# Optimization experiments

Hardware: AMD Instinct MI355X
Metric: run time of the kernel (lower is better)

Reference implementation:

```python
import jax, jax.numpy as jnp
import numpy as np

V_EN = 50000; V_FR = 50000; D = 256; B = 64; S = 64; NEG = 8192; PAD = 0


def setup_inputs() -> dict:
    key = jax.random.key(0)
    k = jax.random.split(key, 8)
    zs = jax.random.normal(k[0], (B, S, D), dtype=jnp.float32) * 0.1
    x_en = jax.random.randint(k[1], (B, S), 1, V_EN)  # avoid pad row 0
    x_fr = jax.random.randint(k[2], (B, S), 1, V_FR)
    en_mask = jnp.ones((B, S), dtype=jnp.float32)
    fr_mask = jnp.ones((B, S), dtype=jnp.float32)
    W_en = jax.random.normal(k[3], (V_EN, D), dtype=jnp.float32) * 0.05
    W_en = W_en.at[PAD].set(0.0)  # padding_idx row is zero
    W_fr = jax.random.normal(k[4], (V_FR, D), dtype=jnp.float32) * 0.05
    W_fr = W_fr.at[PAD].set(0.0)
    # Host-side CSS sampling, mirroring the torch module's numpy/multinomial step.
    rng = np.random.default_rng(0)
    pos_en = np.unique(np.asarray(x_en))
    neg_en = rng.choice(np.setdiff1d(np.arange(V_EN), pos_en), NEG, replace=False)
    kappa_en = jnp.float32((V_EN - pos_en.shape[0]) / NEG)
    pos_fr = np.unique(np.asarray(x_fr))
    neg_fr = rng.choice(np.setdiff1d(np.arange(V_FR), pos_fr), NEG, replace=False)
    kappa_fr = jnp.float32((V_FR - pos_fr.shape[0]) / NEG)
    return {
        "zs": zs, "x_en": x_en, "x_fr": x_fr,
        "en_mask": en_mask, "fr_mask": fr_mask,
        "W_en": W_en, "W_fr": W_fr,
        "pos_en": jnp.asarray(pos_en), "neg_en": jnp.asarray(neg_en),
        "pos_fr": jnp.asarray(pos_fr), "neg_fr": jnp.asarray(neg_fr),
        "kappa_en": kappa_en, "kappa_fr": kappa_fr,
    }


def _css_denom(zs, W, pos_idx, neg_idx, kappa):
    # zs: [B,S,D]; pos/neg embeddings: [P,D]/[N,D] -> denom [B,S]
    pos_e = W[pos_idx]
    neg_e = W[neg_idx]
    pos_score = jnp.exp(jnp.einsum("bsd,pd->bsp", zs, pos_e)).sum(-1)
    neg_score = kappa * jnp.exp(jnp.einsum("bsd,nd->bsn", zs, neg_e)).sum(-1)
    return pos_score + neg_score


def reference(zs, x_en, x_fr, en_mask, fr_mask, W_en, W_fr,
              pos_en, neg_en, pos_fr, neg_fr, kappa_en, kappa_fr):
    # --- English CSS: per-token score ---
    be_en = W_en[x_en]                                   # [B,S,D]
    en_batch = jnp.exp((zs * be_en).sum(-1))             # [B,S]
    en_probs = en_batch / _css_denom(zs, W_en, pos_en, neg_en, kappa_en)
    # --- French CSS: alignment score against every en position ---
    be_fr = W_fr[x_fr]                                   # [B,Sf,D]
    fr_batch = jnp.exp(jnp.einsum("bfd,bsd->bfs", be_fr, zs))  # [B,Sf,S]
    fr_denom = _css_denom(zs, W_fr, pos_fr, neg_fr, kappa_fr)  # [B,S]
    fr_probs = fr_batch / fr_denom[:, None, :]
    en_rec_loss = (jnp.log(en_probs) * en_mask).sum(axis=1)            # [B]
    fr_rec_loss = (jnp.log(fr_probs.sum(axis=2)) * fr_mask).sum(axis=1)  # [B]
    return en_rec_loss, fr_rec_loss
```

## Files before the change

### kernel.cpp

```cpp
#include <hip/hip_runtime.h>

#define DDIM 256
#define NTOK 4096
#define NEGN 8192
#define LOG2E 1.4426950408889634f
#define TM 64
#define TN 64
#define LDT 40

typedef __attribute__((ext_vector_type(8))) short bf16x8;
typedef __attribute__((ext_vector_type(4))) float f32x4;

__device__ inline unsigned short f2bf(float f) {
    unsigned int u = __float_as_uint(f);
    unsigned int r = u + 0x7FFFu + ((u >> 16) & 1u);
    return (unsigned short)(r >> 16);
}

__device__ inline float exp2fast(float x) {
    float r;
    asm("v_exp_f32 %0, %1" : "=v"(r) : "v"(x));
    return r;
}

__device__ inline void gl_lds16(const unsigned short* g, unsigned short* l) {
    __builtin_amdgcn_global_load_lds(
        reinterpret_cast<__attribute__((address_space(1))) unsigned int*>(
            reinterpret_cast<uintptr_t>(g)),
        reinterpret_cast<__attribute__((address_space(3))) unsigned int*>(
            reinterpret_cast<uintptr_t>(l)),
        16, 0, 0);
}

__device__ inline void wait_vmcnt0() { asm volatile("s_waitcnt vmcnt(0)" ::: "memory"); }
__device__ inline void raw_barrier() { asm volatile("s_barrier" ::: "memory"); }

template<int CTRL>
__device__ inline float dpp_add(float x) {
    int v = __builtin_amdgcn_update_dpp(0, __float_as_int(x), CTRL, 0xF, 0xF, false);
    return x + __int_as_float(v);
}
__device__ inline float red16(float x) {
    x = dpp_add<0xB1>(x);
    x = dpp_add<0x4E>(x);
    x = dpp_add<0x141>(x);
    x = dpp_add<0x140>(x);
    return x;
}

__global__ void gather_kernel(
    const float* __restrict__ zs,
    const float* __restrict__ W_en, const float* __restrict__ W_fr,
    const int* __restrict__ pos_en, const int* __restrict__ neg_en,
    const int* __restrict__ pos_fr, const int* __restrict__ neg_fr,
    const int* __restrict__ x_en,
    unsigned short* __restrict__ z_bf,
    unsigned short* __restrict__ E_en, unsigned short* __restrict__ E_fr,
    float* __restrict__ en_score,
    float* __restrict__ denom_en, float* __restrict__ denom_fr,
    int Pe, int Pf, int Lpe, int Lpf)
{
    int row  = blockIdx.x * 4 + (threadIdx.x >> 6);
    int lane = threadIdx.x & 63;
    const float* src = nullptr;
    unsigned short* dst = nullptr;
    bool zero = false;
    float sc = LOG2E;

    if (row < NTOK) {
        src = zs + (size_t)row * DDIM;
        dst = z_bf + (size_t)row * DDIM;
        sc = 1.0f;
        if (lane == 0) { denom_en[row] = 0.0f; denom_fr[row] = 0.0f; }
    } else if (row < NTOK + Lpe) {
        int j = row - NTOK;
        int Le = Pe + NEGN;
        int idx = 0;
        if (j < Pe)      idx = pos_en[j];
        else if (j < Le) idx = neg_en[j - Pe];
        else             zero = true;
        src = W_en + (size_t)idx * DDIM;
        dst = E_en + (size_t)j * DDIM;
    } else if (row < NTOK + Lpe + Lpf) {
        int j = row - NTOK - Lpe;
        int Lf = Pf + NEGN;
        int idx = 0;
        if (j < Pf)      idx = pos_fr[j];
        else if (j < Lf) idx = neg_fr[j - Pf];
        else             zero = true;
        src = W_fr + (size_t)idx * DDIM;
        dst = E_fr + (size_t)j * DDIM;
    } else if (row < NTOK + Lpe + Lpf + NTOK) {
        int j = row - NTOK - Lpe - Lpf;
        int idx = x_en[j];
        float4 z = *(const float4*)(zs   + (size_t)j   * DDIM + lane * 4);
        float4 w = *(const float4*)(W_en + (size_t)idx * DDIM + lane * 4);
        float s = z.x * w.x + z.y * w.y + z.z * w.z + z.w * w.w;
        #pragma unroll
        for (int m = 32; m; m >>= 1) s += __shfl_xor(s, m);
        if (lane == 0) en_score[j] = s;
        return;
    } else {
        return;
    }

    int d = lane * 4;
    float4 v;
    if (zero) { v.x = v.y = v.z = v.w = 0.0f; }
    else      { v = *(const float4*)(src + d); }
    ushort4 o;
    o.x = f2bf(v.x * sc); o.y = f2bf(v.y * sc);
    o.z = f2bf(v.z * sc); o.w = f2bf(v.w * sc);
    *(ushort4*)(dst + d) = o;
}

__global__ __launch_bounds__(512, 4) void expsum_stream(
    const unsigned short* __restrict__ A,
    const unsigned short* __restrict__ E,
    const float* __restrict__ kep, const float* __restrict__ kfp,
    float* __restrict__ out_en, float* __restrict__ out_fr,
    int Pe, int Pf, int Lpe, int NT)
{
    __shared__ __align__(16) unsigned short Bs[2][32 * 512];

    int lin = blockIdx.y * 64 + blockIdx.x;
    int xcd = lin & 7;
    int xb  = (lin >> 3) & 15;
    int sl  = xcd + 8 * (lin >> 7);

    int t    = threadIdx.x;
    int lane = t & 63;
    int wave = t >> 6;
    int col  = lane & 15;
    int quad = lane >> 4;

    float ke = kep[0], kf = kfp[0];
    asm volatile("" : "+v"(ke), "+v"(kf) : : "memory");

    bf16x8 afr[2][8];
    {
        const unsigned short* Ap =
            A + ((size_t)(xb * 256 + wave * 32 + col)) * DDIM + quad * 8;
        #pragma unroll
        for (int i = 0; i < 2; i++)
            #pragma unroll
            for (int c = 0; c < 8; c++)
                afr[i][c] = *(const bf16x8*)(Ap + (size_t)i * 16 * DDIM + c * 32);
    }

    float sums[2][4];
    #pragma unroll
    for (int i = 0; i < 2; i++)
        #pragma unroll
        for (int rr = 0; rr < 4; rr++) sums[i][rr] = 0.0f;

    f32x4 accA[2], accB[2];
    #pragma unroll
    for (int i = 0; i < 2; i++) accB[i] = (f32x4){0.f, 0.f, 0.f, 0.f};
    float wjP = 0.0f;
    float* curout = out_en;
    int outrow = xb * 256 + wave * 32;

    int ntiles = (NT - sl + 31) >> 5;

    #define STAGE_TILE(s) do {                                               \
        int tl_ = sl + ((s) << 5);                                           \
        const unsigned short* g_ =                                           \
            E + (size_t)(tl_ * 64 + lane) * DDIM + wave * 32;                \
        unsigned short* l_ = &Bs[(s) & 1][(wave * 4) * 512];                 \
        _Pragma("unroll")                                                    \
        for (int d_ = 0; d_ < 4; d_++)                                       \
            gl_lds16(g_ + d_ * 8, l_ + d_ * 512);                            \
    } while (0)

    #define J_SWEEP(J, ACCC, ACCD, WJD) do {                                 \
        _Pragma("unroll")                                                    \
        for (int i = 0; i < 2; i++) ACCC[i] = (f32x4){0.f, 0.f, 0.f, 0.f};   \
        _Pragma("unroll")                                                    \
        for (int k8 = 0; k8 < 8; k8++) {                                     \
            bf16x8 bfv = *(const bf16x8*)(                                   \
                &Bs[s & 1][(k8 * 4 + quad) * 512 + ((J) * 16 + col) * 8]);   \
            ACCC[0] = __builtin_amdgcn_mfma_f32_16x16x32_bf16(               \
                afr[0][k8], bfv, ACCC[0], 0, 0, 0);                          \
            ACCC[1] = __builtin_amdgcn_mfma_f32_16x16x32_bf16(               \
                afr[1][k8], bfv, ACCC[1], 0, 0, 0);                          \
            sums[k8 >> 2][k8 & 3] +=                                         \
                (WJD) * exp2fast(ACCD[k8 >> 2][k8 & 3]);                     \
        }                                                                    \
    } while (0)

    #define FLUSH_SUMS() do {                                                \
        _Pragma("unroll")                                                    \
        for (int i = 0; i < 2; i++)                                          \
            _Pragma("unroll")                                                \
            for (int rr = 0; rr < 4; rr++) {                                 \
                float v = red16(sums[i][rr]);                                \
                if (col == 0)                                                \
                    atomicAdd(curout + outrow + 16 * i + quad * 4 + rr, v);  \
                sums[i][rr] = 0.0f;                                          \
            }                                                                \
    } while (0)

    STAGE_TILE(0);

    for (int s = 0; s < ntiles; s++) {
        int tl = sl + (s << 5);
        int nb = tl * 64;

        wait_vmcnt0();
        raw_barrier();

        if (s + 1 < ntiles) STAGE_TILE(s + 1);

        float wj[4];
        #pragma unroll
        for (int j = 0; j < 4; j++) {
            int ngl = nb + 16 * j + col;
            if (nb < Lpe) {
                wj[j] = (ngl < Pe) ? 1.0f : ((ngl < Pe + NEGN) ? ke : 0.0f);
            } else {
                int nl = ngl - Lpe;
                wj[j] = (nl < Pf) ? 1.0f : ((nl < Pf + NEGN) ? kf : 0.0f);
            }
        }
        float* outC = (nb >= Lpe) ? out_fr : out_en;

        J_SWEEP(0, accA, accB, wjP);
        if (outC != curout) {
            FLUSH_SUMS();
            curout = outC;
        }
        J_SWEEP(1, accB, accA, wj[0]);
        J_SWEEP(2, accA, accB, wj[1]);
        J_SWEEP(3, accB, accA, wj[2]);
        wjP = wj[3];
    }
    #undef STAGE_TILE
    #undef J_SWEEP

    #pragma unroll
    for (int i = 0; i < 2; i++)
        #pragma unroll
        for (int rr = 0; rr < 4; rr++)
            sums[i][rr] += wjP * exp2fast(accB[i][rr]);
    FLUSH_SUMS();
    #undef FLUSH_SUMS
}

__global__ __launch_bounds__(256) void expsum_gemm64_loss(
    const float* __restrict__ W_fr,
    const int* __restrict__ x_fr,
    const unsigned short* __restrict__ Bm,
    const float* __restrict__ denom_fr,
    const float* __restrict__ denom_en,
    const float* __restrict__ en_score,
    const float* __restrict__ en_mask,
    const float* __restrict__ fr_mask,
    float* __restrict__ outloss)
{
    __shared__ __align__(16) unsigned short lda[TM * LDT];
    __shared__ __align__(16) unsigned short ldb[TN * LDT];
    __shared__ float tbuf[64];

    int batch = blockIdx.x;
    const unsigned short* Bb = Bm + (size_t)batch * TN * DDIM;

    int t      = threadIdx.x;
    int srow   = t >> 2;
    int schunk = t & 3;
    int lane   = t & 63;
    int wave   = t >> 6;
    int col    = lane & 15;
    int quad   = lane >> 4;

    int aidx = x_fr[batch * 64 + srow];
    const float* Arow = W_fr + (size_t)aidx * DDIM;

    f32x4 acc0 = {0.f,0.f,0.f,0.f};
    f32x4 acc1 = {0.f,0.f,0.f,0.f};
    f32x4 acc2 = {0.f,0.f,0.f,0.f};
    f32x4 acc3 = {0.f,0.f,0.f,0.f};

    for (int kk = 0; kk < DDIM; kk += 32) {
        float4 f0 = *(const float4*)(Arow + kk + schunk * 8);
        float4 f1 = *(const float4*)(Arow + kk + schunk * 8 + 4);
        uint4 bv = *(const uint4*)(Bb + (size_t)srow * DDIM + kk + schunk * 8);
        ushort4 ua; ua.x = f2bf(f0.x * LOG2E); ua.y = f2bf(f0.y * LOG2E);
                    ua.z = f2bf(f0.z * LOG2E); ua.w = f2bf(f0.w * LOG2E);
        ushort4 ub; ub.x = f2bf(f1.x * LOG2E); ub.y = f2bf(f1.y * LOG2E);
                    ub.z = f2bf(f1.z * LOG2E); ub.w = f2bf(f1.w * LOG2E);
        __syncthreads();
        *(ushort4*)(lda + srow * LDT + schunk * 8)     = ua;
        *(ushort4*)(lda + srow * LDT + schunk * 8 + 4) = ub;
        *(uint4*)(ldb + srow * LDT + schunk * 8) = bv;
        __syncthreads();

        bf16x8 af = *(const bf16x8*)(lda + (wave * 16 + col) * LDT + quad * 8);
        bf16x8 b0 = *(const bf16x8*)(ldb + ( 0 + col) * LDT + quad * 8);
        bf16x8 b1 = *(const bf16x8*)(ldb + (16 + col) * LDT + quad * 8);
        bf16x8 b2 = *(const bf16x8*)(ldb + (32 + col) * LDT + quad * 8);
        bf16x8 b3 = *(const bf16x8*)(ldb + (48 + col) * LDT + quad * 8);
        acc0 = __builtin_amdgcn_mfma_f32_16x16x32_bf16(af, b0, acc0, 0, 0, 0);
        acc1 = __builtin_amdgcn_mfma_f32_16x16x32_bf16(af, b1, acc1, 0, 0, 0);
        acc2 = __builtin_amdgcn_mfma_f32_16x16x32_bf16(af, b2, acc2, 0, 0, 0);
        acc3 = __builtin_amdgcn_mfma_f32_16x16x32_bf16(af, b3, acc3, 0, 0, 0);
    }

    const float* db = denom_fr + batch * 64;
    float w0 = 1.0f / db[ 0 + col];
    float w1 = 1.0f / db[16 + col];
    float w2 = 1.0f / db[32 + col];
    float w3 = 1.0f / db[48 + col];

    float tot0 = w0 * exp2fast(acc0.x) + w1 * exp2fast(acc1.x) + w2 * exp2fast(acc2.x) + w3 * exp2fast(acc3.x);
    float tot1 = w0 * exp2fast(acc0.y) + w1 * exp2fast(acc1.y) + w2 * exp2fast(acc2.y) + w3 * exp2fast(acc3.y);
    float tot2 = w0 * exp2fast(acc0.z) + w1 * exp2fast(acc1.z) + w2 * exp2fast(acc2.z) + w3 * exp2fast(acc3.z);
    float tot3 = w0 * exp2fast(acc0.w) + w1 * exp2fast(acc1.w) + w2 * exp2fast(acc2.w) + w3 * exp2fast(acc3.w);

    #pragma unroll
    for (int m = 1; m < 16; m <<= 1) {
        tot0 += __shfl_xor(tot0, m);
        tot1 += __shfl_xor(tot1, m);
        tot2 += __shfl_xor(tot2, m);
        tot3 += __shfl_xor(tot3, m);
    }
    if (col == 0) {
        int base = wave * 16 + quad * 4;
        tbuf[base + 0] = tot0; tbuf[base + 1] = tot1;
        tbuf[base + 2] = tot2; tbuf[base + 3] = tot3;
    }
    __syncthreads();

    if (t < 64) {
        int i = batch * 64 + t;
        float a = (en_score[i] - __logf(denom_en[i])) * en_mask[i];
        float c = __logf(tbuf[t]) * fr_mask[i];
        #pragma unroll
        for (int m = 32; m; m >>= 1) { a += __shfl_xor(a, m); c += __shfl_xor(c, m); }
        if (t == 0) { outloss[batch] = a; outloss[64 + batch] = c; }
    }
}

extern "C" void kernel_launch(void* const* d_in, const int* in_sizes, int n_in,
                              void* d_out, int out_size, void* d_ws, size_t ws_size,
                              hipStream_t stream)
{
    const float* zs       = (const float*)d_in[0];
    const int*   x_en     = (const int*)d_in[1];
    const int*   x_fr     = (const int*)d_in[2];
    const float* en_mask  = (const float*)d_in[3];
    const float* fr_mask  = (const float*)d_in[4];
    const float* W_en     = (const float*)d_in[5];
    const float* W_fr     = (const float*)d_in[6];
    const int*   pos_en   = (const int*)d_in[7];
    const int*   neg_en   = (const int*)d_in[8];
    const int*   pos_fr   = (const int*)d_in[9];
    const int*   neg_fr   = (const int*)d_in[10];
    const float* kappa_en = (const float*)d_in[11];
    const float* kappa_fr = (const float*)d_in[12];

    int Pe  = in_sizes[7];
    int Pf  = in_sizes[9];
    int Lpe = (Pe + NEGN + 63) & ~63;
    int Lpf = (Pf + NEGN + 63) & ~63;
    int Ltot = Lpe + Lpf;
    int NT   = Ltot / 64;

    char* w = (char*)d_ws;
    float* denom_en = (float*)w; w += NTOK * 4;
    float* denom_fr = (float*)w; w += NTOK * 4;
    float* en_score = (float*)w; w += NTOK * 4;
    unsigned short* z_bf  = (unsigned short*)w; w += (size_t)NTOK * DDIM * 2;
    unsigned short* E_all = (unsigned short*)w; w += (size_t)Ltot * DDIM * 2;

    int totrows = NTOK + Lpe + Lpf + NTOK;
    gather_kernel<<<(totrows + 3) / 4, 256, 0, stream>>>(
        zs, W_en, W_fr, pos_en, neg_en, pos_fr, neg_fr, x_en,
        z_bf, E_all, E_all + (size_t)Lpe * DDIM,
        en_score, denom_en, denom_fr, Pe, Pf, Lpe, Lpf);

    expsum_stream<<<dim3(64, 8), 512, 0, stream>>>(
        z_bf, E_all, kappa_en, kappa_fr, denom_en, denom_fr, Pe, Pf, Lpe, NT);

    expsum_gemm64_loss<<<64, 256, 0, stream>>>(
        W_fr, x_fr, z_bf, denom_fr, denom_en, en_score, en_mask, fr_mask,
        (float*)d_out);
}
```

Before: 200.7 us.

## Retile expsum_stream to 128-row blocks with 32-column tiles and 768 blocks

The streaming exp-sum GEMM now uses 256-thread blocks that each own 128 z rows instead of 512-thread blocks owning 256 rows. Each step streams 32 negative/positive embedding columns instead of 64, in a new LDS layout loaded cooperatively by 4 waves. The grid grows to 768 blocks, with a stride of 24 tiles across slices. This aims to improve occupancy and load balance across CUs, at the cost of re-reading each E tile for more row groups and paying barrier overhead per smaller tile.

```diff
diff --git a/kernel.cpp b/kernel.cpp
--- a/kernel.cpp
+++ b/kernel.cpp
@@ -114,19 +114,20 @@
     *(ushort4*)(dst + d) = o;
 }
 
-__global__ __launch_bounds__(512, 4) void expsum_stream(
+__global__ __launch_bounds__(256, 3) void expsum_stream(
     const unsigned short* __restrict__ A,
     const unsigned short* __restrict__ E,
     const float* __restrict__ kep, const float* __restrict__ kfp,
     float* __restrict__ out_en, float* __restrict__ out_fr,
     int Pe, int Pf, int Lpe, int NT)
 {
-    __shared__ __align__(16) unsigned short Bs[2][32 * 512];
+    __shared__ __align__(16) unsigned short Bs[2][8192];
 
     int lin = blockIdx.y * 64 + blockIdx.x;
     int xcd = lin & 7;
-    int xb  = (lin >> 3) & 15;
-    int sl  = xcd + 8 * (lin >> 7);
+    int g3  = lin >> 3;
+    int sl  = xcd + 8 * (g3 % 3);
+    int mg  = g3 / 3;
 
     int t    = threadIdx.x;
     int lane = t & 63;
@@ -140,7 +141,7 @@
     bf16x8 afr[2][8];
     {
         const unsigned short* Ap =
-            A + ((size_t)(xb * 256 + wave * 32 + col)) * DDIM + quad * 8;
+            A + ((size_t)(mg * 128 + wave * 32 + col)) * DDIM + quad * 8;
         #pragma unroll
         for (int i = 0; i < 2; i++)
             #pragma unroll
@@ -159,18 +160,20 @@
     for (int i = 0; i < 2; i++) accB[i] = (f32x4){0.f, 0.f, 0.f, 0.f};
     float wjP = 0.0f;
     float* curout = out_en;
-    int outrow = xb * 256 + wave * 32;
-
-    int ntiles = (NT - sl + 31) >> 5;
+    int outrow = mg * 128 + wave * 32;
+
+    int ntiles = (NT - sl + 23) / 24;
 
     #define STAGE_TILE(s) do {                                               \
-        int tl_ = sl + ((s) << 5);                                           \
+        int tl_ = sl + (s) * 24;                                             \
+        int sub_ = wave & 1;                                                 \
+        int c0_  = (wave >> 1) * 4;                                          \
         const unsigned short* g_ =                                           \
-            E + (size_t)(tl_ * 64 + lane) * DDIM + wave * 32;                \
-        unsigned short* l_ = &Bs[(s) & 1][(wave * 4) * 512];                 \
+            E + (size_t)(tl_ * 32 + sub_ * 16 + col) * DDIM + quad * 8;      \
+        unsigned short* l_ = &Bs[(s) & 1][sub_ * 512];                       \
         _Pragma("unroll")                                                    \
         for (int d_ = 0; d_ < 4; d_++)                                       \
-            gl_lds16(g_ + d_ * 8, l_ + d_ * 512);                            \
+            gl_lds16(g_ + (c0_ + d_) * 32, l_ + (c0_ + d_) * 1024);          \
     } while (0)
 
     #define J_SWEEP(J, ACCC, ACCD, WJD) do {                                 \
@@ -179,7 +182,7 @@
         _Pragma("unroll")                                                    \
         for (int k8 = 0; k8 < 8; k8++) {                                     \
             bf16x8 bfv = *(const bf16x8*)(                                   \
-                &Bs[s & 1][(k8 * 4 + quad) * 512 + ((J) * 16 + col) * 8]);   \
+                &Bs[s & 1][k8 * 1024 + (J) * 512 + quad * 128 + col * 8]);   \
             ACCC[0] = __builtin_amdgcn_mfma_f32_16x16x32_bf16(               \
                 afr[0][k8], bfv, ACCC[0], 0, 0, 0);                          \
             ACCC[1] = __builtin_amdgcn_mfma_f32_16x16x32_bf16(               \
@@ -204,17 +207,17 @@
     STAGE_TILE(0);
 
     for (int s = 0; s < ntiles; s++) {
-        int tl = sl + (s << 5);
-        int nb = tl * 64;
+        int tl = sl + s * 24;
+        int nb = tl * 32;
 
         wait_vmcnt0();
         raw_barrier();
 
         if (s + 1 < ntiles) STAGE_TILE(s + 1);
 
-        float wj[4];
-        #pragma unroll
-        for (int j = 0; j < 4; j++) {
+        float wj[2];
+        #pragma unroll
+        for (int j = 0; j < 2; j++) {
             int ngl = nb + 16 * j + col;
             if (nb < Lpe) {
                 wj[j] = (ngl < Pe) ? 1.0f : ((ngl < Pe + NEGN) ? ke : 0.0f);
@@ -231,9 +234,7 @@
             curout = outC;
         }
         J_SWEEP(1, accB, accA, wj[0]);
-        J_SWEEP(2, accA, accB, wj[1]);
-        J_SWEEP(3, accB, accA, wj[2]);
-        wjP = wj[3];
+        wjP = wj[1];
     }
     #undef STAGE_TILE
     #undef J_SWEEP
@@ -364,7 +365,7 @@
     int Lpe = (Pe + NEGN + 63) & ~63;
     int Lpf = (Pf + NEGN + 63) & ~63;
     int Ltot = Lpe + Lpf;
-    int NT   = Ltot / 64;
+    int NT32 = Ltot / 32;
 
     char* w = (char*)d_ws;
     float* denom_en = (float*)w; w += NTOK * 4;
@@ -379,8 +380,8 @@
         z_bf, E_all, E_all + (size_t)Lpe * DDIM,
         en_score, denom_en, denom_fr, Pe, Pf, Lpe, Lpf);
 
-    expsum_stream<<<dim3(64, 8), 512, 0, stream>>>(
-        z_bf, E_all, kappa_en, kappa_fr, denom_en, denom_fr, Pe, Pf, Lpe, NT);
+    expsum_stream<<<dim3(64, 12), 256, 0, stream>>>(
+        z_bf, E_all, kappa_en, kappa_fr, denom_en, denom_fr, Pe, Pf, Lpe, NT32);
 
     expsum_gemm64_loss<<<64, 256, 0, stream>>>(
         W_fr, x_fr, z_bf, denom_fr, denom_en, en_score, en_mask, fr_mask,
```

New measurement: 198.3 us. Within noise of the previous version (-1.2%).
